# Kernel optimization log

Measured on AMD Instinct MI355X. Metric: run time of the kernel, lower is better.

## Reference

```python
import jax, jax.numpy as jnp
import numpy as np

N_NODES = 100000
N_EDGES = 3200000
F_IN, F_HID, F_OUT = 512, 16, 64


def gcn_conv(x, src, dst, W, b, n):
    # Linear transform first (PyG GCNConv: x @ W, then normalized aggregation, then + bias)
    xw = x @ W  # [n, f_out]
    # symmetric normalization with self-loops (gcn_norm, improved=False)
    deg = jax.ops.segment_sum(jnp.ones_like(dst, dtype=xw.dtype), dst, num_segments=n)
    deg_inv_sqrt = jnp.where(deg > 0, jax.lax.rsqrt(jnp.maximum(deg, 1e-12)), 0.0)
    norm = deg_inv_sqrt[src] * deg_inv_sqrt[dst]  # [E+n]
    out = jax.ops.segment_sum(norm[:, None] * xw[src], dst, num_segments=n)
    return out + b


def setup_inputs() -> dict:
    key = jax.random.key(0)
    k1, k2, k3, k4, k5, k6 = jax.random.split(key, 6)
    x = jax.random.normal(k1, (N_NODES, F_IN), dtype=jnp.float32)
    edge_index = jax.random.randint(k2, (2, N_EDGES), 0, N_NODES, dtype=jnp.int64)
    # Glorot init like PyG GCNConv
    s1 = (6.0 / (F_IN + F_HID)) ** 0.5
    s2 = (6.0 / (F_HID + F_OUT)) ** 0.5
    W1 = jax.random.uniform(k3, (F_IN, F_HID), jnp.float32, -s1, s1)
    b1 = jnp.zeros((F_HID,), jnp.float32)
    W2 = jax.random.uniform(k4, (F_HID, F_OUT), jnp.float32, -s2, s2)
    b2 = jnp.zeros((F_OUT,), jnp.float32)
    return {"x": x, "edge_index": edge_index, "W1": W1, "b1": b1, "W2": W2, "b2": b2}


def reference(x, edge_index, W1, b1, W2, b2):
    n = x.shape[0]
    loop = jnp.arange(n, dtype=edge_index.dtype)
    src = jnp.concatenate([edge_index[0], loop])
    dst = jnp.concatenate([edge_index[1], loop])
    h = jax.nn.relu(gcn_conv(x, src, dst, W1, b1, n))
    out = jax.nn.relu(gcn_conv(h, src, dst, W2, b2, n))
    return out
```

## Files before the change

### kernel.cpp

```cpp
#include <hip/hip_runtime.h>

constexpr int NN   = 100000;
constexpr int NE   = 3200000;
constexpr int FIN  = 512;
constexpr int FH   = 16;
constexpr int FOUT = 64;

constexpr int BSH = 6;
constexpr int BSZ = 64;
constexpr int K   = (NN + BSZ - 1) / BSZ;
constexpr int NB  = 512;
constexpr int CHUNK = NE / NB;
constexpr int CAP = 4096;

__global__ __launch_bounds__(256) void k_cnt(const int* __restrict__ ei, int* __restrict__ M) {
    __shared__ int h[K];
    int t = threadIdx.x, b = blockIdx.x;
    for (int i = t; i < K; i += 256) h[i] = 0;
    __syncthreads();
    int e0 = b * CHUNK;
    for (int e = e0 + t; e < e0 + CHUNK; e += 256)
        atomicAdd(&h[ei[NE + e] >> BSH], 1);
    __syncthreads();
    for (int i = t; i < K; i += 256) M[i * NB + b] = h[i];
}

__global__ __launch_bounds__(256) void k_scanM(int* __restrict__ M, int* __restrict__ btot) {
    int k = blockIdx.x, t = threadIdx.x;
    int2* row = (int2*)(M + (size_t)k * NB);
    int2 v = row[t];
    int s = v.x + v.y;
    int lane = t & 63, wid = t >> 6;
    int ps = s;
    #pragma unroll
    for (int off = 1; off < 64; off <<= 1) {
        int u = __shfl_up(ps, off, 64);
        if (lane >= off) ps += u;
    }
    __shared__ int wsum[4];
    if (lane == 63) wsum[wid] = ps;
    __syncthreads();
    int base = 0;
    for (int w = 0; w < wid; ++w) base += wsum[w];
    int excl = base + ps - s;
    int2 o; o.x = excl; o.y = excl + v.x;
    row[t] = o;
    if (t == 255) btot[k] = excl + s;
}

__global__ __launch_bounds__(1024) void k_scanB(const int* __restrict__ btot, int* __restrict__ bstart) {
    int t = threadIdx.x;
    int i0 = 2 * t, i1 = 2 * t + 1;
    int c0 = (i0 < K) ? btot[i0] : 0;
    int c1 = (i1 < K) ? btot[i1] : 0;
    int s = c0 + c1;
    int lane = t & 63, wid = t >> 6;
    int ps = s;
    #pragma unroll
    for (int off = 1; off < 64; off <<= 1) {
        int u = __shfl_up(ps, off, 64);
        if (lane >= off) ps += u;
    }
    __shared__ int wsum[16];
    if (lane == 63) wsum[wid] = ps;
    __syncthreads();
    int base = 0;
    for (int w = 0; w < wid; ++w) base += wsum[w];
    int excl = base + ps - s;
    if (i0 < K) bstart[i0] = excl;
    if (i1 < K) bstart[i1] = excl + c0;
    if (t == 0) bstart[K] = NE;
}

__global__ __launch_bounds__(256) void k_scatter2(const int* __restrict__ ei,
                                                  const int* __restrict__ M,
                                                  const int* __restrict__ bstart,
                                                  int* __restrict__ rec) {
    __shared__ int cur[K];
    int t = threadIdx.x, b = blockIdx.x;
    for (int i = t; i < K; i += 256) cur[i] = bstart[i] + M[i * NB + b];
    __syncthreads();
    int e0 = b * CHUNK;
    for (int e = e0 + t; e < e0 + CHUNK; e += 256) {
        int s = ei[e];
        int d = ei[NE + e];
        int pos = atomicAdd(&cur[d >> BSH], 1);
        rec[pos] = (s << BSH) | (d & (BSZ - 1));
    }
}

__global__ __launch_bounds__(256) void k_sort2(const int* __restrict__ rec1,
                                               const int* __restrict__ bstart,
                                               int* __restrict__ rec2,
                                               int* __restrict__ row_ptr,
                                               float* __restrict__ dis) {
    __shared__ int h[BSZ];
    __shared__ int cur[BSZ];
    int t = threadIdx.x, k = blockIdx.x;
    if (t < BSZ) h[t] = 0;
    __syncthreads();
    int e0 = bstart[k], e1 = bstart[k + 1];
    for (int e = e0 + t; e < e1; e += 256)
        atomicAdd(&h[rec1[e] & (BSZ - 1)], 1);
    __syncthreads();
    if (t < BSZ) {
        int c = h[t];
        int ps = c;
        #pragma unroll
        for (int off = 1; off < 64; off <<= 1) {
            int u = __shfl_up(ps, off, 64);
            if (t >= off) ps += u;
        }
        int excl = ps - c;
        cur[t] = excl;
        int node = k * BSZ + t;
        if (node < NN) {
            row_ptr[node] = e0 + excl;
            dis[node] = rsqrtf((float)c + 1.0f);
        }
    }
    __syncthreads();
    for (int e = e0 + t; e < e1; e += 256) {
        int r = rec1[e];
        int pos = atomicAdd(&cur[r & (BSZ - 1)], 1);
        rec2[e0 + pos] = r;
    }
    if (k == 0 && t == 0) row_ptr[NN] = NE;
}

__global__ __launch_bounds__(256) void k_gemm1(const float* __restrict__ x,
                                               const float* __restrict__ W1,
                                               const float* __restrict__ dis,
                                               float* __restrict__ vp1) {
    __shared__ float ws[128 * FH];
    __shared__ float xs[64 * 132];
    int t = threadIdx.x;
    int row0 = blockIdx.x * 64;
    int r  = t >> 2;
    int jb = (t & 3) * 4;
    float acc0 = 0.f, acc1 = 0.f, acc2 = 0.f, acc3 = 0.f;

    for (int kc = 0; kc < 4; ++kc) {
        __syncthreads();
        {
            const float* wsrc = &W1[kc * 128 * FH];
            *(float4*)&ws[t * 4]        = *(const float4*)&wsrc[t * 4];
            *(float4*)&ws[1024 + t * 4] = *(const float4*)&wsrc[1024 + t * 4];
        }
        for (int it = 0; it < 8; ++it) {
            int idx = it * 1024 + t * 4;
            int rr = idx >> 7;
            int cc = idx & 127;
            int gr = row0 + rr; if (gr >= NN) gr = NN - 1;
            *(float4*)&xs[rr * 132 + cc] = *(const float4*)&x[(size_t)gr * FIN + kc * 128 + cc];
        }
        __syncthreads();
        const float* xrow = &xs[r * 132];
        #pragma unroll 8
        for (int k = 0; k < 128; ++k) {
            float xv = xrow[k];
            float4 w = *(const float4*)&ws[k * FH + jb];
            acc0 += xv * w.x; acc1 += xv * w.y; acc2 += xv * w.z; acc3 += xv * w.w;
        }
    }
    int node = row0 + r;
    if (node < NN) {
        float d = dis[node];
        *(float4*)&vp1[node * FH + jb] = make_float4(d*acc0, d*acc1, d*acc2, d*acc3);
    }
}

__device__ __forceinline__ float4 seg_gather(const int* __restrict__ recs,
                                             const int* __restrict__ gsrc,
                                             int a, int b, int nst,
                                             const float* __restrict__ vp, int q) {
    float4 acc = make_float4(0.f, 0.f, 0.f, 0.f);
    int blds = b < nst ? b : nst;
    int i = a;
    for (; i + 4 <= blds; i += 4) {
        int r0 = recs[i], r1 = recs[i + 1], r2 = recs[i + 2], r3 = recs[i + 3];
        float4 v0 = *(const float4*)&vp[(r0 >> BSH) * FH + q * 4];
        float4 v1 = *(const float4*)&vp[(r1 >> BSH) * FH + q * 4];
        float4 v2 = *(const float4*)&vp[(r2 >> BSH) * FH + q * 4];
        float4 v3 = *(const float4*)&vp[(r3 >> BSH) * FH + q * 4];
        acc.x += v0.x + v1.x + v2.x + v3.x;
        acc.y += v0.y + v1.y + v2.y + v3.y;
        acc.z += v0.z + v1.z + v2.z + v3.z;
        acc.w += v0.w + v1.w + v2.w + v3.w;
    }
    for (; i < blds; ++i) {
        int r0 = recs[i];
        float4 v0 = *(const float4*)&vp[(r0 >> BSH) * FH + q * 4];
        acc.x += v0.x; acc.y += v0.y; acc.z += v0.z; acc.w += v0.w;
    }
    for (int j = (a > nst ? a : nst); j < b; ++j) {
        int r0 = gsrc[j];
        float4 v0 = *(const float4*)&vp[(r0 >> BSH) * FH + q * 4];
        acc.x += v0.x; acc.y += v0.y; acc.z += v0.z; acc.w += v0.w;
    }
    return acc;
}

__global__ __launch_bounds__(256) void k_agg1(const int* __restrict__ rec2,
                                              const int* __restrict__ bstart,
                                              const int* __restrict__ row_ptr,
                                              const float* __restrict__ dis,
                                              const float* __restrict__ vp1,
                                              const float* __restrict__ b1,
                                              float* __restrict__ vp2) {
    __shared__ int recs[CAP];
    int t = threadIdx.x, k = blockIdx.x;
    int e0 = bstart[k], e1 = bstart[k + 1];
    int len = e1 - e0;
    int nst = len < CAP ? len : CAP;
    for (int i = t; i < nst; i += 256) recs[i] = rec2[e0 + i];
    __syncthreads();
    int slot = t >> 2, q = t & 3;
    int node = k * BSZ + slot;
    if (node >= NN) return;
    int a = row_ptr[node] - e0;
    int b = row_ptr[node + 1] - e0;
    float4 acc = seg_gather(recs, rec2 + e0, a, b, nst, vp1, q);
    float dv = dis[node];
    float4 self = *(const float4*)&vp1[node * FH + q * 4];
    float4 bb   = *(const float4*)&b1[q * 4];
    float4 o;
    o.x = dv * fmaxf(dv * (acc.x + self.x) + bb.x, 0.f);
    o.y = dv * fmaxf(dv * (acc.y + self.y) + bb.y, 0.f);
    o.z = dv * fmaxf(dv * (acc.z + self.z) + bb.z, 0.f);
    o.w = dv * fmaxf(dv * (acc.w + self.w) + bb.w, 0.f);
    *(float4*)&vp2[node * FH + q * 4] = o;
}

__global__ __launch_bounds__(256) void k_agg2(const int* __restrict__ rec2,
                                              const int* __restrict__ bstart,
                                              const int* __restrict__ row_ptr,
                                              const float* __restrict__ dis,
                                              const float* __restrict__ vp2,
                                              const float* __restrict__ W2,
                                              const float* __restrict__ b2,
                                              float* __restrict__ out) {
    __shared__ int   recs[CAP];
    __shared__ float a16[BSZ * FH];
    __shared__ float ws[FH * FOUT];
    int t = threadIdx.x, k = blockIdx.x;
    *(float4*)&ws[t * 4] = *(const float4*)&W2[t * 4];
    int e0 = bstart[k], e1 = bstart[k + 1];
    int len = e1 - e0;
    int nst = len < CAP ? len : CAP;
    for (int i = t; i < nst; i += 256) recs[i] = rec2[e0 + i];
    __syncthreads();
    int slot = t >> 2, q = t & 3;
    int node = k * BSZ + slot;
    float4 r = make_float4(0.f, 0.f, 0.f, 0.f);
    if (node < NN) {
        int a = row_ptr[node] - e0;
        int b = row_ptr[node + 1] - e0;
        float4 acc = seg_gather(recs, rec2 + e0, a, b, nst, vp2, q);
        float dv = dis[node];
        float4 self = *(const float4*)&vp2[node * FH + q * 4];
        r.x = dv * (acc.x + self.x);
        r.y = dv * (acc.y + self.y);
        r.z = dv * (acc.z + self.z);
        r.w = dv * (acc.w + self.w);
    }
    *(float4*)&a16[slot * FH + q * 4] = r;
    __syncthreads();
    int j = t & 63;
    float bj = b2[j];
    float wreg[FH];
    #pragma unroll
    for (int kk = 0; kk < FH; ++kk) wreg[kk] = ws[kk * FOUT + j];
    for (int n = t >> 6; n < BSZ; n += 4) {
        int node2 = k * BSZ + n;
        if (node2 >= NN) break;
        const float* ar = &a16[n * FH];
        float s = 0.f;
        #pragma unroll
        for (int kk = 0; kk < FH; ++kk) s += ar[kk] * wreg[kk];
        out[node2 * FOUT + j] = fmaxf(s + bj, 0.f);
    }
}

extern "C" void kernel_launch(void* const* d_in, const int* in_sizes, int n_in,
                              void* d_out, int out_size, void* d_ws, size_t ws_size,
                              hipStream_t stream) {
    const float* x  = (const float*)d_in[0];
    const int*   ei = (const int*)d_in[1];
    const float* W1 = (const float*)d_in[2];
    const float* b1 = (const float*)d_in[3];
    const float* W2 = (const float*)d_in[4];
    const float* b2 = (const float*)d_in[5];
    float* out = (float*)d_out;

    char* p = (char*)d_ws;
    int*   M       = (int*)p;    p += (size_t)K * NB * 4;
    int*   btot    = (int*)p;    p += 2048 * 4;
    int*   bstart  = (int*)p;    p += 2048 * 4;
    char*  bufA    = p;          p += (size_t)NE * 4;
    int*   rec2    = (int*)p;    p += (size_t)NE * 4;
    int*   row_ptr = (int*)p;    p += 100032 * 4;
    float* dis     = (float*)p;  p += 100032 * 4;

    int*   rec1 = (int*)bufA;
    float* vp1  = (float*)bufA;
    float* vp2  = (float*)(bufA + (size_t)NN * FH * 4);

    k_cnt     <<<NB, 256, 0, stream>>>(ei, M);
    k_scanM   <<<K, 256, 0, stream>>>(M, btot);
    k_scanB   <<<1, 1024, 0, stream>>>(btot, bstart);
    k_scatter2<<<NB, 256, 0, stream>>>(ei, M, bstart, rec1);
    k_sort2   <<<K, 256, 0, stream>>>(rec1, bstart, rec2, row_ptr, dis);

    k_gemm1   <<<(NN + 63) / 64, 256, 0, stream>>>(x, W1, dis, vp1);
    k_agg1    <<<K, 256, 0, stream>>>(rec2, bstart, row_ptr, dis, vp1, b1, vp2);
    k_agg2    <<<K, 256, 0, stream>>>(rec2, bstart, row_ptr, dis, vp2, W2, b2, out);
}
```

Measured before the change: 476.5 us.

## Build CSR via global atomics histogram/scatter and rewrite GEMM as per-thread rows

Replaces the two-level bucketed counting sort (per-block histograms, matrix scan, bucket scatter, intra-bucket sort) with a global atomic degree histogram, a two-kernel scan that also writes row_ptr and dis, and a global atomic scatter that writes source ids straight into CSR order. The first GEMM now gives each thread one full node row with 16 register accumulators, reading W1 directly instead of tiling through shared memory. The gather loop is unrolled to 8 and records store plain source indices. This cuts sort passes and launches but adds heavy global atomic contention, leaves edges within a row in nondeterministic order, and the GEMM uses uncoalesced per-thread row reads.

Measured after the change: 852.5 us. 1.79x slower.

```diff
diff --git a/kernel.cpp b/kernel.cpp
--- a/kernel.cpp
+++ b/kernel.cpp
@@ -6,32 +6,52 @@
 constexpr int FH   = 16;
 constexpr int FOUT = 64;
 
-constexpr int BSH = 6;
-constexpr int BSZ = 64;
-constexpr int K   = (NN + BSZ - 1) / BSZ;
-constexpr int NB  = 512;
-constexpr int CHUNK = NE / NB;
-constexpr int CAP = 4096;
-
-__global__ __launch_bounds__(256) void k_cnt(const int* __restrict__ ei, int* __restrict__ M) {
-    __shared__ int h[K];
-    int t = threadIdx.x, b = blockIdx.x;
-    for (int i = t; i < K; i += 256) h[i] = 0;
-    __syncthreads();
-    int e0 = b * CHUNK;
-    for (int e = e0 + t; e < e0 + CHUNK; e += 256)
-        atomicAdd(&h[ei[NE + e] >> BSH], 1);
-    __syncthreads();
-    for (int i = t; i < K; i += 256) M[i * NB + b] = h[i];
-}
-
-__global__ __launch_bounds__(256) void k_scanM(int* __restrict__ M, int* __restrict__ btot) {
-    int k = blockIdx.x, t = threadIdx.x;
-    int2* row = (int2*)(M + (size_t)k * NB);
-    int2 v = row[t];
-    int s = v.x + v.y;
+constexpr int BSZ  = 64;
+constexpr int K    = (NN + BSZ - 1) / BSZ;
+constexpr int CAP  = 4096;
+constexpr int NNP  = 100352;
+
+__global__ __launch_bounds__(256) void k_zero(int* __restrict__ deg) {
+    int i = blockIdx.x * 256 + threadIdx.x;
+    if (i < NN / 4) ((int4*)deg)[i] = make_int4(0, 0, 0, 0);
+}
+
+__global__ __launch_bounds__(256) void k_hist(const int* __restrict__ ei, int* __restrict__ deg) {
+    int i = blockIdx.x * 256 + threadIdx.x;
+    int4 d = ((const int4*)(ei + NE))[i];
+    atomicAdd(&deg[d.x], 1);
+    atomicAdd(&deg[d.y], 1);
+    atomicAdd(&deg[d.z], 1);
+    atomicAdd(&deg[d.w], 1);
+}
+
+__global__ __launch_bounds__(256) void k_red(const int* __restrict__ deg, int* __restrict__ bsum) {
+    int b = blockIdx.x, t = threadIdx.x;
+    int gi = b * 1024 + 4 * t;
+    int s = 0;
+    if (gi < NN) { int4 d = *(const int4*)&deg[gi]; s = d.x + d.y + d.z + d.w; }
+    #pragma unroll
+    for (int off = 32; off; off >>= 1) s += __shfl_down(s, off, 64);
+    __shared__ int w[4];
+    if ((t & 63) == 0) w[t >> 6] = s;
+    __syncthreads();
+    if (t == 0) bsum[b] = w[0] + w[1] + w[2] + w[3];
+}
+
+__global__ __launch_bounds__(256) void k_scan3(const int* __restrict__ deg,
+                                               const int* __restrict__ bsum,
+                                               int* __restrict__ row_ptr,
+                                               int* __restrict__ cur,
+                                               float* __restrict__ dis) {
+    int b = blockIdx.x, t = threadIdx.x;
+    int cb = 0;
+    for (int j = 0; j < b; ++j) cb += bsum[j];
+    int gi = b * 1024 + 4 * t;
+    int4 d = make_int4(0, 0, 0, 0);
+    if (gi < NN) d = *(const int4*)&deg[gi];
+    int ts = d.x + d.y + d.z + d.w;
     int lane = t & 63, wid = t >> 6;
-    int ps = s;
+    int ps = ts;
     #pragma unroll
     for (int off = 1; off < 64; off <<= 1) {
         int u = __shfl_up(ps, off, 64);
@@ -40,133 +60,63 @@
     __shared__ int wsum[4];
     if (lane == 63) wsum[wid] = ps;
     __syncthreads();
-    int base = 0;
+    int base = cb;
     for (int w = 0; w < wid; ++w) base += wsum[w];
-    int excl = base + ps - s;
-    int2 o; o.x = excl; o.y = excl + v.x;
-    row[t] = o;
-    if (t == 255) btot[k] = excl + s;
-}
-
-__global__ __launch_bounds__(1024) void k_scanB(const int* __restrict__ btot, int* __restrict__ bstart) {
-    int t = threadIdx.x;
-    int i0 = 2 * t, i1 = 2 * t + 1;
-    int c0 = (i0 < K) ? btot[i0] : 0;
-    int c1 = (i1 < K) ? btot[i1] : 0;
-    int s = c0 + c1;
-    int lane = t & 63, wid = t >> 6;
-    int ps = s;
-    #pragma unroll
-    for (int off = 1; off < 64; off <<= 1) {
-        int u = __shfl_up(ps, off, 64);
-        if (lane >= off) ps += u;
-    }
-    __shared__ int wsum[16];
-    if (lane == 63) wsum[wid] = ps;
-    __syncthreads();
-    int base = 0;
-    for (int w = 0; w < wid; ++w) base += wsum[w];
-    int excl = base + ps - s;
-    if (i0 < K) bstart[i0] = excl;
-    if (i1 < K) bstart[i1] = excl + c0;
-    if (t == 0) bstart[K] = NE;
-}
-
-__global__ __launch_bounds__(256) void k_scatter2(const int* __restrict__ ei,
-                                                  const int* __restrict__ M,
-                                                  const int* __restrict__ bstart,
-                                                  int* __restrict__ rec) {
-    __shared__ int cur[K];
-    int t = threadIdx.x, b = blockIdx.x;
-    for (int i = t; i < K; i += 256) cur[i] = bstart[i] + M[i * NB + b];
-    __syncthreads();
-    int e0 = b * CHUNK;
-    for (int e = e0 + t; e < e0 + CHUNK; e += 256) {
-        int s = ei[e];
-        int d = ei[NE + e];
-        int pos = atomicAdd(&cur[d >> BSH], 1);
-        rec[pos] = (s << BSH) | (d & (BSZ - 1));
-    }
-}
-
-__global__ __launch_bounds__(256) void k_sort2(const int* __restrict__ rec1,
-                                               const int* __restrict__ bstart,
-                                               int* __restrict__ rec2,
-                                               int* __restrict__ row_ptr,
-                                               float* __restrict__ dis) {
-    __shared__ int h[BSZ];
-    __shared__ int cur[BSZ];
-    int t = threadIdx.x, k = blockIdx.x;
-    if (t < BSZ) h[t] = 0;
-    __syncthreads();
-    int e0 = bstart[k], e1 = bstart[k + 1];
-    for (int e = e0 + t; e < e1; e += 256)
-        atomicAdd(&h[rec1[e] & (BSZ - 1)], 1);
-    __syncthreads();
-    if (t < BSZ) {
-        int c = h[t];
-        int ps = c;
-        #pragma unroll
-        for (int off = 1; off < 64; off <<= 1) {
-            int u = __shfl_up(ps, off, 64);
-            if (t >= off) ps += u;
-        }
-        int excl = ps - c;
-        cur[t] = excl;
-        int node = k * BSZ + t;
-        if (node < NN) {
-            row_ptr[node] = e0 + excl;
-            dis[node] = rsqrtf((float)c + 1.0f);
-        }
-    }
-    __syncthreads();
-    for (int e = e0 + t; e < e1; e += 256) {
-        int r = rec1[e];
-        int pos = atomicAdd(&cur[r & (BSZ - 1)], 1);
-        rec2[e0 + pos] = r;
-    }
-    if (k == 0 && t == 0) row_ptr[NN] = NE;
+    int r0 = base + ps - ts;
+    if (gi < NN) {
+        int r1 = r0 + d.x, r2 = r1 + d.y, r3 = r2 + d.z;
+        *(int4*)&row_ptr[gi] = make_int4(r0, r1, r2, r3);
+        *(int4*)&cur[gi]     = make_int4(r0, r1, r2, r3);
+        *(float4*)&dis[gi]   = make_float4(rsqrtf((float)d.x + 1.f), rsqrtf((float)d.y + 1.f),
+                                           rsqrtf((float)d.z + 1.f), rsqrtf((float)d.w + 1.f));
+    }
+    if (b == 0 && t == 0) row_ptr[NN] = NE;
+}
+
+__global__ __launch_bounds__(256) void k_scatter(const int* __restrict__ ei,
+                                                 int* __restrict__ cur,
+                                                 int* __restrict__ rec2) {
+    int i = blockIdx.x * 256 + threadIdx.x;
+    int4 s = ((const int4*)ei)[i];
+    int4 d = ((const int4*)(ei + NE))[i];
+    int p0 = atomicAdd(&cur[d.x], 1); rec2[p0] = s.x;
+    int p1 = atomicAdd(&cur[d.y], 1); rec2[p1] = s.y;
+    int p2 = atomicAdd(&cur[d.z], 1); rec2[p2] = s.z;
+    int p3 = atomicAdd(&cur[d.w], 1); rec2[p3] = s.w;
 }
 
 __global__ __launch_bounds__(256) void k_gemm1(const float* __restrict__ x,
                                                const float* __restrict__ W1,
                                                const float* __restrict__ dis,
                                                float* __restrict__ vp1) {
-    __shared__ float ws[128 * FH];
-    __shared__ float xs[64 * 132];
-    int t = threadIdx.x;
-    int row0 = blockIdx.x * 64;
-    int r  = t >> 2;
-    int jb = (t & 3) * 4;
-    float acc0 = 0.f, acc1 = 0.f, acc2 = 0.f, acc3 = 0.f;
-
-    for (int kc = 0; kc < 4; ++kc) {
-        __syncthreads();
-        {
-            const float* wsrc = &W1[kc * 128 * FH];
-            *(float4*)&ws[t * 4]        = *(const float4*)&wsrc[t * 4];
-            *(float4*)&ws[1024 + t * 4] = *(const float4*)&wsrc[1024 + t * 4];
+    int node = blockIdx.x * 256 + threadIdx.x;
+    int n = node < NN ? node : NN - 1;
+    const float* xr = x + (size_t)n * FIN;
+    float acc[FH];
+    #pragma unroll
+    for (int j = 0; j < FH; ++j) acc[j] = 0.f;
+    for (int k0 = 0; k0 < FIN; k0 += 16) {
+        float4 xv[4];
+        #pragma unroll
+        for (int u = 0; u < 4; ++u) xv[u] = *(const float4*)&xr[k0 + 4 * u];
+        #pragma unroll
+        for (int u = 0; u < 4; ++u) {
+            #pragma unroll
+            for (int kk = 0; kk < 4; ++kk) {
+                float xs = ((const float*)&xv[u])[kk];
+                const float* wr = &W1[(k0 + 4 * u + kk) * FH];
+                #pragma unroll
+                for (int j = 0; j < FH; ++j) acc[j] += xs * wr[j];
+            }
         }
-        for (int it = 0; it < 8; ++it) {
-            int idx = it * 1024 + t * 4;
-            int rr = idx >> 7;
-            int cc = idx & 127;
-            int gr = row0 + rr; if (gr >= NN) gr = NN - 1;
-            *(float4*)&xs[rr * 132 + cc] = *(const float4*)&x[(size_t)gr * FIN + kc * 128 + cc];
-        }
-        __syncthreads();
-        const float* xrow = &xs[r * 132];
-        #pragma unroll 8
-        for (int k = 0; k < 128; ++k) {
-            float xv = xrow[k];
-            float4 w = *(const float4*)&ws[k * FH + jb];
-            acc0 += xv * w.x; acc1 += xv * w.y; acc2 += xv * w.z; acc3 += xv * w.w;
-        }
-    }
-    int node = row0 + r;
+    }
     if (node < NN) {
-        float d = dis[node];
-        *(float4*)&vp1[node * FH + jb] = make_float4(d*acc0, d*acc1, d*acc2, d*acc3);
+        float dv = dis[node];
+        #pragma unroll
+        for (int jb = 0; jb < 4; ++jb)
+            *(float4*)&vp1[(size_t)node * FH + jb * 4] =
+                make_float4(dv * acc[jb * 4], dv * acc[jb * 4 + 1],
+                            dv * acc[jb * 4 + 2], dv * acc[jb * 4 + 3]);
     }
 }
 
@@ -177,32 +127,36 @@
     float4 acc = make_float4(0.f, 0.f, 0.f, 0.f);
     int blds = b < nst ? b : nst;
     int i = a;
-    for (; i + 4 <= blds; i += 4) {
-        int r0 = recs[i], r1 = recs[i + 1], r2 = recs[i + 2], r3 = recs[i + 3];
-        float4 v0 = *(const float4*)&vp[(r0 >> BSH) * FH + q * 4];
-        float4 v1 = *(const float4*)&vp[(r1 >> BSH) * FH + q * 4];
-        float4 v2 = *(const float4*)&vp[(r2 >> BSH) * FH + q * 4];
-        float4 v3 = *(const float4*)&vp[(r3 >> BSH) * FH + q * 4];
-        acc.x += v0.x + v1.x + v2.x + v3.x;
-        acc.y += v0.y + v1.y + v2.y + v3.y;
-        acc.z += v0.z + v1.z + v2.z + v3.z;
-        acc.w += v0.w + v1.w + v2.w + v3.w;
+    for (; i + 8 <= blds; i += 8) {
+        int r0 = recs[i],     r1 = recs[i + 1], r2 = recs[i + 2], r3 = recs[i + 3];
+        int r4 = recs[i + 4], r5 = recs[i + 5], r6 = recs[i + 6], r7 = recs[i + 7];
+        float4 v0 = *(const float4*)&vp[(size_t)r0 * FH + q * 4];
+        float4 v1 = *(const float4*)&vp[(size_t)r1 * FH + q * 4];
+        float4 v2 = *(const float4*)&vp[(size_t)r2 * FH + q * 4];
+        float4 v3 = *(const float4*)&vp[(size_t)r3 * FH + q * 4];
+        float4 v4 = *(const float4*)&vp[(size_t)r4 * FH + q * 4];
+        float4 v5 = *(const float4*)&vp[(size_t)r5 * FH + q * 4];
+        float4 v6 = *(const float4*)&vp[(size_t)r6 * FH + q * 4];
+        float4 v7 = *(const float4*)&vp[(size_t)r7 * FH + q * 4];
+        acc.x += ((v0.x + v1.x) + (v2.x + v3.x)) + ((v4.x + v5.x) + (v6.x + v7.x));
+        acc.y += ((v0.y + v1.y) + (v2.y + v3.y)) + ((v4.y + v5.y) + (v6.y + v7.y));
+        acc.z += ((v0.z + v1.z) + (v2.z + v3.z)) + ((v4.z + v5.z) + (v6.z + v7.z));
+        acc.w += ((v0.w + v1.w) + (v2.w + v3.w)) + ((v4.w + v5.w) + (v6.w + v7.w));
     }
     for (; i < blds; ++i) {
         int r0 = recs[i];
-        float4 v0 = *(const float4*)&vp[(r0 >> BSH) * FH + q * 4];
+        float4 v0 = *(const float4*)&vp[(size_t)r0 * FH + q * 4];
         acc.x += v0.x; acc.y += v0.y; acc.z += v0.z; acc.w += v0.w;
     }
     for (int j = (a > nst ? a : nst); j < b; ++j) {
         int r0 = gsrc[j];
-        float4 v0 = *(const float4*)&vp[(r0 >> BSH) * FH + q * 4];
+        float4 v0 = *(const float4*)&vp[(size_t)r0 * FH + q * 4];
         acc.x += v0.x; acc.y += v0.y; acc.z += v0.z; acc.w += v0.w;
     }
     return acc;
 }
 
 __global__ __launch_bounds__(256) void k_agg1(const int* __restrict__ rec2,
-                                              const int* __restrict__ bstart,
                                               const int* __restrict__ row_ptr,
                                               const float* __restrict__ dis,
                                               const float* __restrict__ vp1,
@@ -210,30 +164,30 @@
                                               float* __restrict__ vp2) {
     __shared__ int recs[CAP];
     int t = threadIdx.x, k = blockIdx.x;
-    int e0 = bstart[k], e1 = bstart[k + 1];
-    int len = e1 - e0;
-    int nst = len < CAP ? len : CAP;
+    int n0 = k * BSZ;
+    int nend = n0 + BSZ < NN ? n0 + BSZ : NN;
+    int e0 = row_ptr[n0], e1 = row_ptr[nend];
+    int len = e1 - e0, nst = len < CAP ? len : CAP;
     for (int i = t; i < nst; i += 256) recs[i] = rec2[e0 + i];
     __syncthreads();
     int slot = t >> 2, q = t & 3;
-    int node = k * BSZ + slot;
+    int node = n0 + slot;
     if (node >= NN) return;
     int a = row_ptr[node] - e0;
     int b = row_ptr[node + 1] - e0;
     float4 acc = seg_gather(recs, rec2 + e0, a, b, nst, vp1, q);
     float dv = dis[node];
-    float4 self = *(const float4*)&vp1[node * FH + q * 4];
+    float4 self = *(const float4*)&vp1[(size_t)node * FH + q * 4];
     float4 bb   = *(const float4*)&b1[q * 4];
     float4 o;
     o.x = dv * fmaxf(dv * (acc.x + self.x) + bb.x, 0.f);
     o.y = dv * fmaxf(dv * (acc.y + self.y) + bb.y, 0.f);
     o.z = dv * fmaxf(dv * (acc.z + self.z) + bb.z, 0.f);
     o.w = dv * fmaxf(dv * (acc.w + self.w) + bb.w, 0.f);
-    *(float4*)&vp2[node * FH + q * 4] = o;
+    *(float4*)&vp2[(size_t)node * FH + q * 4] = o;
 }
 
 __global__ __launch_bounds__(256) void k_agg2(const int* __restrict__ rec2,
-                                              const int* __restrict__ bstart,
                                               const int* __restrict__ row_ptr,
                                               const float* __restrict__ dis,
                                               const float* __restrict__ vp2,
@@ -245,20 +199,21 @@
     __shared__ float ws[FH * FOUT];
     int t = threadIdx.x, k = blockIdx.x;
     *(float4*)&ws[t * 4] = *(const float4*)&W2[t * 4];
-    int e0 = bstart[k], e1 = bstart[k + 1];
-    int len = e1 - e0;
-    int nst = len < CAP ? len : CAP;
+    int n0 = k * BSZ;
+    int nend = n0 + BSZ < NN ? n0 + BSZ : NN;
+    int e0 = row_ptr[n0], e1 = row_ptr[nend];
+    int len = e1 - e0, nst = len < CAP ? len : CAP;
     for (int i = t; i < nst; i += 256) recs[i] = rec2[e0 + i];
     __syncthreads();
     int slot = t >> 2, q = t & 3;
-    int node = k * BSZ + slot;
+    int node = n0 + slot;
     float4 r = make_float4(0.f, 0.f, 0.f, 0.f);
     if (node < NN) {
         int a = row_ptr[node] - e0;
         int b = row_ptr[node + 1] - e0;
         float4 acc = seg_gather(recs, rec2 + e0, a, b, nst, vp2, q);
         float dv = dis[node];
-        float4 self = *(const float4*)&vp2[node * FH + q * 4];
+        float4 self = *(const float4*)&vp2[(size_t)node * FH + q * 4];
         r.x = dv * (acc.x + self.x);
         r.y = dv * (acc.y + self.y);
         r.z = dv * (acc.z + self.z);
@@ -272,13 +227,13 @@
     #pragma unroll
     for (int kk = 0; kk < FH; ++kk) wreg[kk] = ws[kk * FOUT + j];
     for (int n = t >> 6; n < BSZ; n += 4) {
-        int node2 = k * BSZ + n;
+        int node2 = n0 + n;
         if (node2 >= NN) break;
         const float* ar = &a16[n * FH];
         float s = 0.f;
         #pragma unroll
         for (int kk = 0; kk < FH; ++kk) s += ar[kk] * wreg[kk];
-        out[node2 * FOUT + j] = fmaxf(s + bj, 0.f);
+        out[(size_t)node2 * FOUT + j] = fmaxf(s + bj, 0.f);
     }
 }
 
@@ -294,25 +249,22 @@
     float* out = (float*)d_out;
 
     char* p = (char*)d_ws;
-    int*   M       = (int*)p;    p += (size_t)K * NB * 4;
-    int*   btot    = (int*)p;    p += 2048 * 4;
-    int*   bstart  = (int*)p;    p += 2048 * 4;
-    char*  bufA    = p;          p += (size_t)NE * 4;
+    int*   deg     = (int*)p;    p += (size_t)NNP * 4;
+    int*   bsum    = (int*)p;    p += 128 * 4;
+    int*   row_ptr = (int*)p;    p += (size_t)(NNP + 4) * 4;
+    int*   cur     = (int*)p;    p += (size_t)NNP * 4;
+    float* dis     = (float*)p;  p += (size_t)NNP * 4;
     int*   rec2    = (int*)p;    p += (size_t)NE * 4;
-    int*   row_ptr = (int*)p;    p += 100032 * 4;
-    float* dis     = (float*)p;  p += 100032 * 4;
-
-    int*   rec1 = (int*)bufA;
-    float* vp1  = (float*)bufA;
-    float* vp2  = (float*)(bufA + (size_t)NN * FH * 4);
-
-    k_cnt     <<<NB, 256, 0, stream>>>(ei, M);
-    k_scanM   <<<K, 256, 0, stream>>>(M, btot);
-    k_scanB   <<<1, 1024, 0, stream>>>(btot, bstart);
-    k_scatter2<<<NB, 256, 0, stream>>>(ei, M, bstart, rec1);
-    k_sort2   <<<K, 256, 0, stream>>>(rec1, bstart, rec2, row_ptr, dis);
-
-    k_gemm1   <<<(NN + 63) / 64, 256, 0, stream>>>(x, W1, dis, vp1);
-    k_agg1    <<<K, 256, 0, stream>>>(rec2, bstart, row_ptr, dis, vp1, b1, vp2);
-    k_agg2    <<<K, 256, 0, stream>>>(rec2, bstart, row_ptr, dis, vp2, W2, b2, out);
-}
+    float* vp1     = (float*)p;  p += (size_t)NN * FH * 4;
+    float* vp2     = (float*)p;
+
+    k_zero   <<<98,   256, 0, stream>>>(deg);
+    k_hist   <<<3125, 256, 0, stream>>>(ei, deg);
+    k_red    <<<98,   256, 0, stream>>>(deg, bsum);
+    k_scan3  <<<98,   256, 0, stream>>>(deg, bsum, row_ptr, cur, dis);
+    k_scatter<<<3125, 256, 0, stream>>>(ei, cur, rec2);
+
+    k_gemm1  <<<(NN + 255) / 256, 256, 0, stream>>>(x, W1, dis, vp1);
+    k_agg1   <<<K, 256, 0, stream>>>(rec2, row_ptr, dis, vp1, b1, vp2);
+    k_agg2   <<<K, 256, 0, stream>>>(rec2, row_ptr, dis, vp2, W2, b2, out);
+}
```

## Rewrite GEMM1 as one-row-per-thread, pre-shift sorted records, unroll gather by 8

Applied to the files above, without the earlier changes.

The first-layer GEMM drops its shared-memory tiling and uses one thread per node. Each thread streams its own x row with float4 loads and keeps all 16 accumulators in registers, while W1 is read through the scalar/cache path. The sort kernel now stores already-shifted source indices, which removes the shift from every gather. The gather loop is unrolled to 8 outstanding loads for more memory-level parallelism. The per-thread row access to x is strided across lanes, so loads are uncoalesced and register pressure goes up.

Measured after the change: 551.9 us. 15.8% more time.

```diff
diff --git a/kernel.cpp b/kernel.cpp
--- a/kernel.cpp
+++ b/kernel.cpp
@@ -123,7 +123,7 @@
     for (int e = e0 + t; e < e1; e += 256) {
         int r = rec1[e];
         int pos = atomicAdd(&cur[r & (BSZ - 1)], 1);
-        rec2[e0 + pos] = r;
+        rec2[e0 + pos] = r >> BSH;
     }
     if (k == 0 && t == 0) row_ptr[NN] = NE;
 }
@@ -132,41 +132,34 @@
                                                const float* __restrict__ W1,
                                                const float* __restrict__ dis,
                                                float* __restrict__ vp1) {
-    __shared__ float ws[128 * FH];
-    __shared__ float xs[64 * 132];
-    int t = threadIdx.x;
-    int row0 = blockIdx.x * 64;
-    int r  = t >> 2;
-    int jb = (t & 3) * 4;
-    float acc0 = 0.f, acc1 = 0.f, acc2 = 0.f, acc3 = 0.f;
-
-    for (int kc = 0; kc < 4; ++kc) {
-        __syncthreads();
-        {
-            const float* wsrc = &W1[kc * 128 * FH];
-            *(float4*)&ws[t * 4]        = *(const float4*)&wsrc[t * 4];
-            *(float4*)&ws[1024 + t * 4] = *(const float4*)&wsrc[1024 + t * 4];
+    int node = blockIdx.x * 256 + threadIdx.x;
+    int n = node < NN ? node : NN - 1;
+    const float* xr = x + (size_t)n * FIN;
+    float acc[FH];
+    #pragma unroll
+    for (int j = 0; j < FH; ++j) acc[j] = 0.f;
+    for (int k0 = 0; k0 < FIN; k0 += 16) {
+        float4 xv[4];
+        #pragma unroll
+        for (int u = 0; u < 4; ++u) xv[u] = *(const float4*)&xr[k0 + 4 * u];
+        #pragma unroll
+        for (int u = 0; u < 4; ++u) {
+            #pragma unroll
+            for (int kk = 0; kk < 4; ++kk) {
+                float xs = ((const float*)&xv[u])[kk];
+                const float* wr = &W1[(k0 + 4 * u + kk) * FH];
+                #pragma unroll
+                for (int j = 0; j < FH; ++j) acc[j] += xs * wr[j];
+            }
         }
-        for (int it = 0; it < 8; ++it) {
-            int idx = it * 1024 + t * 4;
-            int rr = idx >> 7;
-            int cc = idx & 127;
-            int gr = row0 + rr; if (gr >= NN) gr = NN - 1;
-            *(float4*)&xs[rr * 132 + cc] = *(const float4*)&x[(size_t)gr * FIN + kc * 128 + cc];
-        }
-        __syncthreads();
-        const float* xrow = &xs[r * 132];
-        #pragma unroll 8
-        for (int k = 0; k < 128; ++k) {
-            float xv = xrow[k];
-            float4 w = *(const float4*)&ws[k * FH + jb];
-            acc0 += xv * w.x; acc1 += xv * w.y; acc2 += xv * w.z; acc3 += xv * w.w;
-        }
-    }
-    int node = row0 + r;
+    }
     if (node < NN) {
-        float d = dis[node];
-        *(float4*)&vp1[node * FH + jb] = make_float4(d*acc0, d*acc1, d*acc2, d*acc3);
+        float dv = dis[node];
+        #pragma unroll
+        for (int jb = 0; jb < 4; ++jb)
+            *(float4*)&vp1[(size_t)node * FH + jb * 4] =
+                make_float4(dv * acc[jb * 4], dv * acc[jb * 4 + 1],
+                            dv * acc[jb * 4 + 2], dv * acc[jb * 4 + 3]);
     }
 }
 
@@ -177,25 +170,30 @@
     float4 acc = make_float4(0.f, 0.f, 0.f, 0.f);
     int blds = b < nst ? b : nst;
     int i = a;
-    for (; i + 4 <= blds; i += 4) {
-        int r0 = recs[i], r1 = recs[i + 1], r2 = recs[i + 2], r3 = recs[i + 3];
-        float4 v0 = *(const float4*)&vp[(r0 >> BSH) * FH + q * 4];
-        float4 v1 = *(const float4*)&vp[(r1 >> BSH) * FH + q * 4];
-        float4 v2 = *(const float4*)&vp[(r2 >> BSH) * FH + q * 4];
-        float4 v3 = *(const float4*)&vp[(r3 >> BSH) * FH + q * 4];
-        acc.x += v0.x + v1.x + v2.x + v3.x;
-        acc.y += v0.y + v1.y + v2.y + v3.y;
-        acc.z += v0.z + v1.z + v2.z + v3.z;
-        acc.w += v0.w + v1.w + v2.w + v3.w;
+    for (; i + 8 <= blds; i += 8) {
+        int r0 = recs[i],     r1 = recs[i + 1], r2 = recs[i + 2], r3 = recs[i + 3];
+        int r4 = recs[i + 4], r5 = recs[i + 5], r6 = recs[i + 6], r7 = recs[i + 7];
+        float4 v0 = *(const float4*)&vp[(size_t)r0 * FH + q * 4];
+        float4 v1 = *(const float4*)&vp[(size_t)r1 * FH + q * 4];
+        float4 v2 = *(const float4*)&vp[(size_t)r2 * FH + q * 4];
+        float4 v3 = *(const float4*)&vp[(size_t)r3 * FH + q * 4];
+        float4 v4 = *(const float4*)&vp[(size_t)r4 * FH + q * 4];
+        float4 v5 = *(const float4*)&vp[(size_t)r5 * FH + q * 4];
+        float4 v6 = *(const float4*)&vp[(size_t)r6 * FH + q * 4];
+        float4 v7 = *(const float4*)&vp[(size_t)r7 * FH + q * 4];
+        acc.x += ((v0.x + v1.x) + (v2.x + v3.x)) + ((v4.x + v5.x) + (v6.x + v7.x));
+        acc.y += ((v0.y + v1.y) + (v2.y + v3.y)) + ((v4.y + v5.y) + (v6.y + v7.y));
+        acc.z += ((v0.z + v1.z) + (v2.z + v3.z)) + ((v4.z + v5.z) + (v6.z + v7.z));
+        acc.w += ((v0.w + v1.w) + (v2.w + v3.w)) + ((v4.w + v5.w) + (v6.w + v7.w));
     }
     for (; i < blds; ++i) {
         int r0 = recs[i];
-        float4 v0 = *(const float4*)&vp[(r0 >> BSH) * FH + q * 4];
+        float4 v0 = *(const float4*)&vp[(size_t)r0 * FH + q * 4];
         acc.x += v0.x; acc.y += v0.y; acc.z += v0.z; acc.w += v0.w;
     }
     for (int j = (a > nst ? a : nst); j < b; ++j) {
         int r0 = gsrc[j];
-        float4 v0 = *(const float4*)&vp[(r0 >> BSH) * FH + q * 4];
+        float4 v0 = *(const float4*)&vp[(size_t)r0 * FH + q * 4];
         acc.x += v0.x; acc.y += v0.y; acc.z += v0.z; acc.w += v0.w;
     }
     return acc;
@@ -211,8 +209,7 @@
     __shared__ int recs[CAP];
     int t = threadIdx.x, k = blockIdx.x;
     int e0 = bstart[k], e1 = bstart[k + 1];
-    int len = e1 - e0;
-    int nst = len < CAP ? len : CAP;
+    int len = e1 - e0, nst = len < CAP ? len : CAP;
     for (int i = t; i < nst; i += 256) recs[i] = rec2[e0 + i];
     __syncthreads();
     int slot = t >> 2, q = t & 3;
@@ -222,14 +219,14 @@
     int b = row_ptr[node + 1] - e0;
     float4 acc = seg_gather(recs, rec2 + e0, a, b, nst, vp1, q);
     float dv = dis[node];
-    float4 self = *(const float4*)&vp1[node * FH + q * 4];
+    float4 self = *(const float4*)&vp1[(size_t)node * FH + q * 4];
     float4 bb   = *(const float4*)&b1[q * 4];
     float4 o;
     o.x = dv * fmaxf(dv * (acc.x + self.x) + bb.x, 0.f);
     o.y = dv * fmaxf(dv * (acc.y + self.y) + bb.y, 0.f);
     o.z = dv * fmaxf(dv * (acc.z + self.z) + bb.z, 0.f);
     o.w = dv * fmaxf(dv * (acc.w + self.w) + bb.w, 0.f);
-    *(float4*)&vp2[node * FH + q * 4] = o;
+    *(float4*)&vp2[(size_t)node * FH + q * 4] = o;
 }
 
 __global__ __launch_bounds__(256) void k_agg2(const int* __restrict__ rec2,
@@ -246,8 +243,7 @@
     int t = threadIdx.x, k = blockIdx.x;
     *(float4*)&ws[t * 4] = *(const float4*)&W2[t * 4];
     int e0 = bstart[k], e1 = bstart[k + 1];
-    int len = e1 - e0;
-    int nst = len < CAP ? len : CAP;
+    int len = e1 - e0, nst = len < CAP ? len : CAP;
     for (int i = t; i < nst; i += 256) recs[i] = rec2[e0 + i];
     __syncthreads();
     int slot = t >> 2, q = t & 3;
@@ -258,7 +254,7 @@
         int b = row_ptr[node + 1] - e0;
         float4 acc = seg_gather(recs, rec2 + e0, a, b, nst, vp2, q);
         float dv = dis[node];
-        float4 self = *(const float4*)&vp2[node * FH + q * 4];
+        float4 self = *(const float4*)&vp2[(size_t)node * FH + q * 4];
         r.x = dv * (acc.x + self.x);
         r.y = dv * (acc.y + self.y);
         r.z = dv * (acc.z + self.z);
@@ -278,7 +274,7 @@
         float s = 0.f;
         #pragma unroll
         for (int kk = 0; kk < FH; ++kk) s += ar[kk] * wreg[kk];
-        out[node2 * FOUT + j] = fmaxf(s + bj, 0.f);
+        out[(size_t)node2 * FOUT + j] = fmaxf(s + bj, 0.f);
     }
 }
 
@@ -312,7 +308,7 @@
     k_scatter2<<<NB, 256, 0, stream>>>(ei, M, bstart, rec1);
     k_sort2   <<<K, 256, 0, stream>>>(rec1, bstart, rec2, row_ptr, dis);
 
-    k_gemm1   <<<(NN + 63) / 64, 256, 0, stream>>>(x, W1, dis, vp1);
+    k_gemm1   <<<(NN + 255) / 256, 256, 0, stream>>>(x, W1, dis, vp1);
     k_agg1    <<<K, 256, 0, stream>>>(rec2, bstart, row_ptr, dis, vp1, b1, vp2);
     k_agg2    <<<K, 256, 0, stream>>>(rec2, bstart, row_ptr, dis, vp2, W2, b2, out);
 }
```
